# Optimization experiments

Measured on AMD Instinct MI355X. Metric: run time of the kernel, lower is better.

The kernel has to match this reference:

```python
import jax, jax.numpy as jnp
import numpy as np

B, T, C = 128, 256, 256
K1, S1, T1 = 2, 2, 128   # conv scale 1: kernel, stride, output time steps
K2, S2, T2 = 4, 4, 64    # conv scale 2
TT = T + T1 + T2         # 448, concatenated time dim fed to TriU
EPS = 1e-5


def hardswish(x):
    return x * jnp.clip(x + 3.0, 0.0, 6.0) / 6.0


def setup_inputs() -> dict:
    key = jax.random.key(0)
    ks = jax.random.split(key, 9)
    return {
        "x": jax.random.normal(ks[0], (B, T, C), jnp.float32),
        "conv_w1": jax.random.normal(ks[1], (C, C, K1), jnp.float32) * 0.05,
        "conv_b1": jax.random.normal(ks[2], (C,), jnp.float32) * 0.05,
        "conv_w2": jax.random.normal(ks[3], (C, C, K2), jnp.float32) * 0.05,
        "conv_b2": jax.random.normal(ks[4], (C,), jnp.float32) * 0.05,
        "ln1_g": jnp.ones((T1, C), jnp.float32),
        "ln1_b": jnp.zeros((T1, C), jnp.float32),
        "ln2_g": jnp.ones((T2, C), jnp.float32),
        "ln2_b": jnp.zeros((T2, C), jnp.float32),
        "triu_w1": jax.random.normal(ks[5], (TT, TT), jnp.float32) * 0.05,
        "triu_b1": jax.random.normal(ks[6], (TT,), jnp.float32) * 0.05,
        "triu_w2": jax.random.normal(ks[7], (TT, TT), jnp.float32) * 0.05,
        "triu_b2": jax.random.normal(ks[8], (TT,), jnp.float32) * 0.05,
    }


def _layernorm2(x, g, b):
    # nn.LayerNorm([ts, C]): normalize jointly over last two dims of [B, ts, C]
    mu = jnp.mean(x, axis=(-2, -1), keepdims=True)
    var = jnp.var(x, axis=(-2, -1), keepdims=True)
    return (x - mu) * jax.lax.rsqrt(var + EPS) * g + b


def _conv1d(x_bct, w, b, stride):
    # x: [B, C, T], w: [Cout, Cin, K] -> [B, Cout, T_out], VALID padding
    y = jax.lax.conv_general_dilated(
        x_bct, w, window_strides=(stride,), padding='VALID',
        dimension_numbers=('NCH', 'OIH', 'NCH'))
    return y + b[None, :, None]


def reference(x, conv_w1, conv_b1, conv_w2, conv_b2,
              ln1_g, ln1_b, ln2_g, ln2_b,
              triu_w1, triu_b1, triu_w2, triu_b2):
    xc = jnp.transpose(x, (0, 2, 1))  # [B, C, T]
    f1 = _layernorm2(jnp.transpose(_conv1d(xc, conv_w1, conv_b1, S1), (0, 2, 1)), ln1_g, ln1_b)
    f2 = _layernorm2(jnp.transpose(_conv1d(xc, conv_w2, conv_b2, S2), (0, 2, 1)), ln2_g, ln2_b)
    cat = jnp.concatenate([x, f1, f2], axis=1)  # [B, TT, C]
    # TriU network on time axis: per-step Linear(i+1,1) == upper-triangular matmul
    z = jnp.transpose(cat, (0, 2, 1))  # [B, C, TT]
    mask = jnp.triu(jnp.ones((TT, TT), z.dtype))  # M[j,i]=w_i[j] for j<=i
    z = hardswish(z @ (triu_w1 * mask) + triu_b1)
    z = z @ (triu_w2 * mask) + triu_b2
    return jnp.transpose(z, (0, 2, 1))  # [B, TT, C]
```

## Files before the change

kernel.cpp:

```cpp
#include <hip/hip_runtime.h>
#include <hip/hip_bf16.h>

#define Bn   128
#define Tn   256
#define Cn   256
#define T1n  128
#define T2n  64
#define TTn  448
#define EPSf 1e-5f

typedef __attribute__((ext_vector_type(8))) short short8;
typedef __attribute__((ext_vector_type(4))) short short4v;
typedef __attribute__((ext_vector_type(4))) float f32x4;

__device__ __forceinline__ unsigned short f2b(float f) {
    union { __hip_bfloat16 h; unsigned short u; } cv;
    cv.h = __float2bfloat16(f);
    return cv.u;
}

__device__ __forceinline__ short8 cvt8(float4 a, float4 b) {
    short8 r;
    r[0] = (short)f2b(a.x); r[1] = (short)f2b(a.y); r[2] = (short)f2b(a.z); r[3] = (short)f2b(a.w);
    r[4] = (short)f2b(b.x); r[5] = (short)f2b(b.y); r[6] = (short)f2b(b.z); r[7] = (short)f2b(b.w);
    return r;
}

__global__ __launch_bounds__(256) void prep_all(
        const float* __restrict__ cw1, const float* __restrict__ cw2,
        const float* __restrict__ tw1, const float* __restrict__ tw2,
        const float* __restrict__ ln1g, const float* __restrict__ ln1b,
        const float* __restrict__ ln2g, const float* __restrict__ ln2b,
        unsigned short* __restrict__ w1rT, unsigned short* __restrict__ w2rT,
        unsigned short* __restrict__ wm1b, unsigned short* __restrict__ wm2b,
        float* __restrict__ gt1, float* __restrict__ bt1,
        float* __restrict__ gt2, float* __restrict__ bt2) {
    int idx = blockIdx.x * 256 + threadIdx.x;
    if (idx < 131072) {
        int co = idx >> 9, r = idx & 511, k = r >> 8, ci = r & 255;
        w1rT[idx] = f2b(cw1[(size_t)co * 512 + ci * 2 + k]);
    } else if ((idx -= 131072) < 262144) {
        int co = idx >> 10, r = idx & 1023, k = r >> 8, ci = r & 255;
        w2rT[idx] = f2b(cw2[(size_t)co * 1024 + ci * 4 + k]);
    } else if ((idx -= 262144) < 200704) {
        int i = idx / TTn, j = idx % TTn;
        wm1b[idx] = (j <= i) ? f2b(tw1[(size_t)j * TTn + i]) : (unsigned short)0;
    } else if ((idx -= 200704) < 200704) {
        int i = idx / TTn, j = idx % TTn;
        wm2b[idx] = (j <= i) ? f2b(tw2[(size_t)j * TTn + i]) : (unsigned short)0;
    } else if ((idx -= 200704) < 32768) {
        int c = idx >> 7, r = idx & 127;
        gt1[idx] = ln1g[(size_t)r * Cn + c];
    } else if ((idx -= 32768) < 32768) {
        int c = idx >> 7, r = idx & 127;
        bt1[idx] = ln1b[(size_t)r * Cn + c];
    } else if ((idx -= 32768) < 16384) {
        int c = idx >> 6, r = idx & 63;
        gt2[idx] = ln2g[(size_t)r * Cn + c];
    } else if ((idx -= 16384) < 16384) {
        int c = idx >> 6, r = idx & 63;
        bt2[idx] = ln2b[(size_t)r * Cn + c];
    }
}

__global__ __launch_bounds__(256) void xpose_kernel(const float* __restrict__ x,
                                                    unsigned short* __restrict__ catb) {
    __shared__ float tl[64][65];
    int b = blockIdx.z, t0 = blockIdx.y * 64, c0 = blockIdx.x * 64;
    const float* xp = x + (size_t)b * Tn * Cn;
    int lr = threadIdx.x >> 4;
    int lc = (threadIdx.x & 15) * 4;
#pragma unroll
    for (int rr = 0; rr < 4; ++rr) {
        int row = lr + rr * 16;
        float4 v = *(const float4*)(xp + (size_t)(t0 + row) * Cn + c0 + lc);
        tl[lc + 0][row] = v.x; tl[lc + 1][row] = v.y;
        tl[lc + 2][row] = v.z; tl[lc + 3][row] = v.w;
    }
    __syncthreads();
    int cr = threadIdx.x >> 2, tq = (threadIdx.x & 3) * 16;
    unsigned short* qp = catb + (size_t)b * (TTn * Cn) + (size_t)(c0 + cr) * TTn + t0 + tq;
    short8 o0, o1;
#pragma unroll
    for (int j = 0; j < 8; ++j) {
        o0[j] = (short)f2b(tl[cr][tq + j]);
        o1[j] = (short)f2b(tl[cr][tq + 8 + j]);
    }
    *(short8*)(qp) = o0;
    *(short8*)(qp + 8) = o1;
}

__device__ __forceinline__ void conv_body(char* smem,
        const float* __restrict__ x, int lda,
        const unsigned short* __restrict__ Bw,
        const float* __restrict__ bias,
        float* __restrict__ Cout, long cstride, int ldc, int K,
        float* __restrict__ psout, int slot, int nslots,
        int m0, int n0, int bz) {
    const int tid = threadIdx.x;
    const int lane = tid & 63;
    const int wid = tid >> 6;
    const int wr = wid >> 1, wc = wid & 1;

    const int ar = tid >> 2, akq = tid & 3;
    const int bn_ = tid >> 1, bkh = (tid & 1) * 32;

    const float* Afp = x + (size_t)bz * (Tn * Cn) + (size_t)(m0 + ar) * lda + akq * 16;
    const unsigned short* Bp = Bw + (size_t)(n0 + bn_) * K + bkh;

    const int awb = ar * 128 + akq * 32;
    const int aswz = (ar & 7) << 4;
    const int bwb = bn_ * 128 + bkh * 2;
    const int bswz = (bn_ & 7) << 4;

    short8 ra0, ra1, rb0, rb1, rb2, rb3;
    auto loadA = [&](int k0) {
        const float* p = Afp + k0;
        float4 v0 = *(const float4*)(p);
        float4 v1 = *(const float4*)(p + 4);
        float4 v2 = *(const float4*)(p + 8);
        float4 v3 = *(const float4*)(p + 12);
        ra0 = cvt8(v0, v1);
        ra1 = cvt8(v2, v3);
    };
    auto loadB = [&](int k0) {
        rb0 = *(const short8*)(Bp + k0);
        rb1 = *(const short8*)(Bp + k0 + 8);
        rb2 = *(const short8*)(Bp + k0 + 16);
        rb3 = *(const short8*)(Bp + k0 + 24);
    };
    auto stage = [&](int buf) {
        char* AsB = smem + buf * 8192;
        char* BsB = smem + 16384 + buf * 16384;
        *(short8*)(AsB + ((awb) ^ aswz)) = ra0;
        *(short8*)(AsB + ((awb + 16) ^ aswz)) = ra1;
        *(short8*)(BsB + ((bwb) ^ bswz)) = rb0;
        *(short8*)(BsB + ((bwb + 16) ^ bswz)) = rb1;
        *(short8*)(BsB + ((bwb + 32) ^ bswz)) = rb2;
        *(short8*)(BsB + ((bwb + 48) ^ bswz)) = rb3;
    };

    const int fl = lane & 15;
    const int fkb = (lane >> 4) * 16;
    const int amb = (wr * 32 + fl) * 128;
    const int bnb = (wc * 64 + fl) * 128;
    const int fswz = (fl & 7) << 4;

    f32x4 acc[2][4];
#pragma unroll
    for (int i = 0; i < 2; ++i)
#pragma unroll
        for (int j = 0; j < 4; ++j) acc[i][j] = (f32x4){0.f, 0.f, 0.f, 0.f};

    const int nkt = K >> 6;
    loadA(0); loadB(0);
    stage(0);
    __syncthreads();
    for (int kt = 0; kt < nkt; ++kt) {
        const int cur = kt & 1;
        if (kt + 1 < nkt) { loadA((kt + 1) * 64); loadB((kt + 1) * 64); }
        char* AsB = smem + cur * 8192;
        char* BsB = smem + 16384 + cur * 16384;
#pragma unroll
        for (int ks = 0; ks < 2; ++ks) {
            const int kb = ks * 64 + fkb;
            short8 af0 = *(const short8*)(AsB + ((amb + kb) ^ fswz));
            short8 af1 = *(const short8*)(AsB + ((amb + 2048 + kb) ^ fswz));
            short8 bf0 = *(const short8*)(BsB + ((bnb + kb) ^ fswz));
            short8 bf1 = *(const short8*)(BsB + ((bnb + 2048 + kb) ^ fswz));
            short8 bf2 = *(const short8*)(BsB + ((bnb + 4096 + kb) ^ fswz));
            short8 bf3 = *(const short8*)(BsB + ((bnb + 6144 + kb) ^ fswz));
            acc[0][0] = __builtin_amdgcn_mfma_f32_16x16x32_bf16(af0, bf0, acc[0][0], 0, 0, 0);
            acc[0][1] = __builtin_amdgcn_mfma_f32_16x16x32_bf16(af0, bf1, acc[0][1], 0, 0, 0);
            acc[0][2] = __builtin_amdgcn_mfma_f32_16x16x32_bf16(af0, bf2, acc[0][2], 0, 0, 0);
            acc[0][3] = __builtin_amdgcn_mfma_f32_16x16x32_bf16(af0, bf3, acc[0][3], 0, 0, 0);
            acc[1][0] = __builtin_amdgcn_mfma_f32_16x16x32_bf16(af1, bf0, acc[1][0], 0, 0, 0);
            acc[1][1] = __builtin_amdgcn_mfma_f32_16x16x32_bf16(af1, bf1, acc[1][1], 0, 0, 0);
            acc[1][2] = __builtin_amdgcn_mfma_f32_16x16x32_bf16(af1, bf2, acc[1][2], 0, 0, 0);
            acc[1][3] = __builtin_amdgcn_mfma_f32_16x16x32_bf16(af1, bf3, acc[1][3], 0, 0, 0);
        }
        if (kt + 1 < nkt) stage(cur ^ 1);
        __syncthreads();
    }

    const int lrow = (lane >> 4) * 4;
    float s_ = 0.f, ss_ = 0.f;
#pragma unroll
    for (int mf = 0; mf < 2; ++mf) {
        const int trow = m0 + wr * 32 + mf * 16 + lrow;
#pragma unroll
        for (int nf = 0; nf < 4; ++nf) {
            const int col = n0 + wc * 64 + nf * 16 + fl;
            f32x4 v = acc[mf][nf];
            v += bias[col];
#pragma unroll
            for (int r = 0; r < 4; ++r) { s_ += v[r]; ss_ = fmaf(v[r], v[r], ss_); }
            float* Cb = Cout + (size_t)bz * cstride + (size_t)col * ldc + trow;
            *(f32x4*)Cb = v;
        }
    }

#pragma unroll
    for (int o = 32; o > 0; o >>= 1) { s_ += __shfl_down(s_, o); ss_ += __shfl_down(ss_, o); }
    float* rsm = (float*)smem;
    if (lane == 0) { rsm[wid] = s_; rsm[wid + 4] = ss_; }
    __syncthreads();
    if (tid == 0) {
        float S = rsm[0] + rsm[1] + rsm[2] + rsm[3];
        float SS = rsm[4] + rsm[5] + rsm[6] + rsm[7];
        psout[((size_t)bz * nslots + slot) * 2 + 0] = S;
        psout[((size_t)bz * nslots + slot) * 2 + 1] = SS;
    }
}

__global__ __launch_bounds__(256) void conv_all(
        const float* __restrict__ x,
        const unsigned short* __restrict__ w1rT, const unsigned short* __restrict__ w2rT,
        const float* __restrict__ cb1, const float* __restrict__ cb2,
        float* __restrict__ c1t, float* __restrict__ c2t,
        float* __restrict__ ps1, float* __restrict__ ps2) {
    __shared__ alignas(16) char smem[49152];
    const int y = blockIdx.y, xb = blockIdx.x, bz = blockIdx.z;
    if (y < 2) {
        conv_body(smem, x, 512, w1rT, cb1, c1t, (long)Cn * T1n, T1n, 512,
                  ps1, y * 2 + xb, 4, y * 64, xb * 128, bz);
    } else {
        conv_body(smem, x, 1024, w2rT, cb2, c2t, (long)Cn * T2n, T2n, 1024,
                  ps2, xb, 2, 0, xb * 128, bz);
    }
}

__global__ __launch_bounds__(256) void ln_apply_both(
        const float* __restrict__ c1t, const float* __restrict__ c2t,
        const float* __restrict__ gt1, const float* __restrict__ bt1,
        const float* __restrict__ gt2, const float* __restrict__ bt2,
        const float* __restrict__ ps1, const float* __restrict__ ps2,
        unsigned short* __restrict__ catb) {
    const int b = blockIdx.y, bx = blockIdx.x;
    const float *p, *g, *be;
    unsigned short* q;
    int LG, n, base;
    float S = 0.f, SS = 0.f;
    if (bx < 16) {
        n = Cn * T1n; LG = 7;
        p = c1t + (size_t)b * n; g = gt1; be = bt1;
        q = catb + (size_t)b * (TTn * Cn) + Tn;
#pragma unroll
        for (int s_ = 0; s_ < 4; ++s_) { S += ps1[b * 8 + s_ * 2]; SS += ps1[b * 8 + s_ * 2 + 1]; }
        base = bx * 2048;
    } else {
        n = Cn * T2n; LG = 6;
        p = c2t + (size_t)b * n; g = gt2; be = bt2;
        q = catb + (size_t)b * (TTn * Cn) + Tn + T1n;
#pragma unroll
        for (int s_ = 0; s_ < 2; ++s_) { S += ps2[b * 4 + s_ * 2]; SS += ps2[b * 4 + s_ * 2 + 1]; }
        base = (bx - 16) * 2048;
    }
    float mu = S / n;
    float rs = rsqrtf(SS / n - mu * mu + EPSf);

    int i = base + threadIdx.x * 8;
    int c = i >> LG, t = i & ((1 << LG) - 1);
    float4 v0 = *(const float4*)(p + i);
    float4 v1 = *(const float4*)(p + i + 4);
    float4 g0 = *(const float4*)(g + i);
    float4 g1 = *(const float4*)(g + i + 4);
    float4 b0 = *(const float4*)(be + i);
    float4 b1 = *(const float4*)(be + i + 4);
    float4 o0, o1;
    o0.x = fmaf((v0.x - mu) * rs, g0.x, b0.x);
    o0.y = fmaf((v0.y - mu) * rs, g0.y, b0.y);
    o0.z = fmaf((v0.z - mu) * rs, g0.z, b0.z);
    o0.w = fmaf((v0.w - mu) * rs, g0.w, b0.w);
    o1.x = fmaf((v1.x - mu) * rs, g1.x, b1.x);
    o1.y = fmaf((v1.y - mu) * rs, g1.y, b1.y);
    o1.z = fmaf((v1.z - mu) * rs, g1.z, b1.z);
    o1.w = fmaf((v1.w - mu) * rs, g1.w, b1.w);
    *(short8*)(q + (size_t)c * TTn + t) = cvt8(o0, o1);
}

template<int EPI>
__global__ __launch_bounds__(256)
void triu_db(const unsigned short* __restrict__ Asrc,
             const unsigned short* __restrict__ Bsrc,
             const float* __restrict__ bias,
             void* __restrict__ Cv) {
    const int tid = threadIdx.x;
    const int lane = tid & 63;
    const int wid = tid >> 6;
    const int wr = wid >> 1, wc = wid & 1;

    const int bid = blockIdx.x;
    const int xcd = bid & 7, seq = bid >> 3;
    const int m0 = (seq % 7) * 64;
    const long n0 = (long)(xcd * 32 + seq / 7) * 128;

    __shared__ unsigned short As[2][64 * 64];
    __shared__ unsigned short Bs[2][128 * 64];

    const int ar = tid >> 2, akq = tid & 3;
    const int bn_ = tid >> 1, bkh = (tid & 1) * 32;

    const unsigned short* Ap = Asrc + (size_t)(m0 + ar) * TTn + akq * 16;
    const unsigned short* Bp = Bsrc + (size_t)(n0 + bn_) * TTn + bkh;

    const int awb = ar * 128 + akq * 32;
    const int aswz = (ar & 7) << 4;
    const int bwb = bn_ * 128 + bkh * 2;
    const int bswz = (bn_ & 7) << 4;

    short8 ra0, ra1, rb[4];
    auto loadAB = [&](int k0) {
        ra0 = *(const short8*)(Ap + k0);
        ra1 = *(const short8*)(Ap + k0 + 8);
#pragma unroll
        for (int j = 0; j < 4; ++j) rb[j] = *(const short8*)(Bp + k0 + j * 8);
    };
    auto stage = [&](int buf) {
        char* AsB = (char*)As[buf];
        char* BsB = (char*)Bs[buf];
        *(short8*)(AsB + ((awb) ^ aswz)) = ra0;
        *(short8*)(AsB + ((awb + 16) ^ aswz)) = ra1;
#pragma unroll
        for (int j = 0; j < 4; ++j)
            *(short8*)(BsB + ((bwb + j * 16) ^ bswz)) = rb[j];
    };

    const int fl = lane & 15;
    const int fkb = (lane >> 4) * 16;
    const int amb = (wr * 32 + fl) * 128;
    const int bnb = (wc * 64 + fl) * 128;
    const int fswz = (fl & 7) << 4;

    f32x4 acc[2][4];
#pragma unroll
    for (int i = 0; i < 2; ++i)
#pragma unroll
        for (int j = 0; j < 4; ++j) acc[i][j] = (f32x4){0.f, 0.f, 0.f, 0.f};

    const int nkt = (m0 >> 6) + 1;

    loadAB(0);
    stage(0);
    __syncthreads();
    for (int kt = 0; kt < nkt; ++kt) {
        const int cur = kt & 1;
        if (kt + 1 < nkt) loadAB((kt + 1) * 64);
        char* AsB = (char*)As[cur];
        char* BsB = (char*)Bs[cur];
#pragma unroll
        for (int ks = 0; ks < 2; ++ks) {
            const int kb = ks * 64 + fkb;
            short8 af0 = *(const short8*)(AsB + ((amb + kb) ^ fswz));
            short8 af1 = *(const short8*)(AsB + ((amb + 2048 + kb) ^ fswz));
            short8 bf0 = *(const short8*)(BsB + ((bnb + kb) ^ fswz));
            short8 bf1 = *(const short8*)(BsB + ((bnb + 2048 + kb) ^ fswz));
            short8 bf2 = *(const short8*)(BsB + ((bnb + 4096 + kb) ^ fswz));
            short8 bf3 = *(const short8*)(BsB + ((bnb + 6144 + kb) ^ fswz));
            acc[0][0] = __builtin_amdgcn_mfma_f32_16x16x32_bf16(af0, bf0, acc[0][0], 0, 0, 0);
            acc[0][1] = __builtin_amdgcn_mfma_f32_16x16x32_bf16(af0, bf1, acc[0][1], 0, 0, 0);
            acc[0][2] = __builtin_amdgcn_mfma_f32_16x16x32_bf16(af0, bf2, acc[0][2], 0, 0, 0);
            acc[0][3] = __builtin_amdgcn_mfma_f32_16x16x32_bf16(af0, bf3, acc[0][3], 0, 0, 0);
            acc[1][0] = __builtin_amdgcn_mfma_f32_16x16x32_bf16(af1, bf0, acc[1][0], 0, 0, 0);
            acc[1][1] = __builtin_amdgcn_mfma_f32_16x16x32_bf16(af1, bf1, acc[1][1], 0, 0, 0);
            acc[1][2] = __builtin_amdgcn_mfma_f32_16x16x32_bf16(af1, bf2, acc[1][2], 0, 0, 0);
            acc[1][3] = __builtin_amdgcn_mfma_f32_16x16x32_bf16(af1, bf3, acc[1][3], 0, 0, 0);
        }
        if (kt + 1 < nkt) stage(cur ^ 1);
        __syncthreads();
    }

    const int lrow = (lane >> 4) * 4;
#pragma unroll
    for (int mf = 0; mf < 2; ++mf) {
        const int trow = m0 + wr * 32 + mf * 16 + lrow;
        f32x4 bv = *(const f32x4*)(bias + trow);
#pragma unroll
        for (int nf = 0; nf < 4; ++nf) {
            const long coln = n0 + wc * 64 + nf * 16 + fl;
            f32x4 v = acc[mf][nf] + bv;
            if (EPI == 1) {
                unsigned short* Cb = (unsigned short*)Cv + (size_t)coln * TTn + trow;
                short4v pk;
#pragma unroll
                for (int r = 0; r < 4; ++r) {
                    float t = v[r];
                    float u = fminf(fmaxf(t + 3.f, 0.f), 6.f);
                    t = t * u * (1.f / 6.f);
                    pk[r] = (short)f2b(t);
                }
                *(short4v*)Cb = pk;
            } else {
                const int b = (int)(coln >> 8), c = (int)(coln & 255);
                float* Cb = (float*)Cv + ((size_t)b * TTn + trow) * Cn + c;
#pragma unroll
                for (int r = 0; r < 4; ++r) Cb[(size_t)r * Cn] = v[r];
            }
        }
    }
}

extern "C" void kernel_launch(void* const* d_in, const int* in_sizes, int n_in,
                              void* d_out, int out_size, void* d_ws, size_t ws_size,
                              hipStream_t stream) {
    const float* x    = (const float*)d_in[0];
    const float* cw1  = (const float*)d_in[1];
    const float* cb1  = (const float*)d_in[2];
    const float* cw2  = (const float*)d_in[3];
    const float* cb2  = (const float*)d_in[4];
    const float* ln1g = (const float*)d_in[5];
    const float* ln1b = (const float*)d_in[6];
    const float* ln2g = (const float*)d_in[7];
    const float* ln2b = (const float*)d_in[8];
    const float* tw1  = (const float*)d_in[9];
    const float* tb1  = (const float*)d_in[10];
    const float* tw2  = (const float*)d_in[11];
    const float* tb2  = (const float*)d_in[12];
    float* out = (float*)d_out;

    char* w = (char*)d_ws;
    unsigned short* catb = (unsigned short*)w;
    unsigned short* z1b  = (unsigned short*)(w + 29360128);
    float*          c1t  = (float*)(w + 58720256);
    float*          c2t  = (float*)(w + 75497472);
    unsigned short* w1rT = (unsigned short*)(w + 83886080);
    unsigned short* w2rT = (unsigned short*)(w + 84148224);
    unsigned short* wm1b = (unsigned short*)(w + 84672512);
    unsigned short* wm2b = (unsigned short*)(w + 85073920);
    float*          gt1  = (float*)(w + 85475328);
    float*          bt1  = (float*)(w + 85606400);
    float*          gt2  = (float*)(w + 85737472);
    float*          bt2  = (float*)(w + 85803008);
    float*          ps1  = (float*)(w + 85868544);
    float*          ps2  = (float*)(w + 85872640);

    prep_all<<<3488, 256, 0, stream>>>(cw1, cw2, tw1, tw2, ln1g, ln1b, ln2g, ln2b,
                                       w1rT, w2rT, wm1b, wm2b, gt1, bt1, gt2, bt2);

    xpose_kernel<<<dim3(4, 4, Bn), 256, 0, stream>>>(x, catb);

    conv_all<<<dim3(2, 3, Bn), 256, 0, stream>>>(x, w1rT, w2rT, cb1, cb2, c1t, c2t, ps1, ps2);

    ln_apply_both<<<dim3(24, Bn), 256, 0, stream>>>(c1t, c2t, gt1, bt1, gt2, bt2, ps1, ps2, catb);

    triu_db<1><<<1792, 256, 0, stream>>>(wm1b, catb, tb1, z1b);

    triu_db<2><<<1792, 256, 0, stream>>>(wm2b, z1b, tb2, out);
}
```

Before: 99.11 us.

## Fuse all stages into one persistent cooperative kernel with grid syncs

Replaces six separate kernel launches with one cooperative persistent kernel that loops over virtual block indices for each stage and separates the stages with grid-wide barriers. The goal is to remove per-launch overhead and inter-kernel gaps. In exchange, occupancy is capped by the shared 48KB smem and the launch-bounds hint, the triu GEMM and conv units now run with a limited resident grid and lose the XCD mapping implied by hardware block order, and device property queries are added on the host side of every launch.

Result: slower. 266.6 us (+169.0%).

```diff
diff --git a/kernel.cpp b/kernel.cpp
--- a/kernel.cpp
+++ b/kernel.cpp
@@ -1,5 +1,8 @@
 #include <hip/hip_runtime.h>
 #include <hip/hip_bf16.h>
+#include <hip/hip_cooperative_groups.h>
+
+namespace cg = cooperative_groups;
 
 #define Bn   128
 #define Tn   256
@@ -13,6 +16,13 @@
 typedef __attribute__((ext_vector_type(4))) short short4v;
 typedef __attribute__((ext_vector_type(4))) float f32x4;
 
+struct Params {
+    const float *x, *cw1, *cb1, *cw2, *cb2, *ln1g, *ln1b, *ln2g, *ln2b, *tw1, *tb1, *tw2, *tb2;
+    float* out;
+    unsigned short *catb, *z1b, *w1rT, *w2rT, *wm1b, *wm2b;
+    float *c1t, *c2t, *gt1, *bt1, *gt2, *bt2, *ps1, *ps2;
+};
+
 __device__ __forceinline__ unsigned short f2b(float f) {
     union { __hip_bfloat16 h; unsigned short u; } cv;
     cv.h = __float2bfloat16(f);
@@ -26,48 +36,40 @@
     return r;
 }
 
-__global__ __launch_bounds__(256) void prep_all(
-        const float* __restrict__ cw1, const float* __restrict__ cw2,
-        const float* __restrict__ tw1, const float* __restrict__ tw2,
-        const float* __restrict__ ln1g, const float* __restrict__ ln1b,
-        const float* __restrict__ ln2g, const float* __restrict__ ln2b,
-        unsigned short* __restrict__ w1rT, unsigned short* __restrict__ w2rT,
-        unsigned short* __restrict__ wm1b, unsigned short* __restrict__ wm2b,
-        float* __restrict__ gt1, float* __restrict__ bt1,
-        float* __restrict__ gt2, float* __restrict__ bt2) {
-    int idx = blockIdx.x * 256 + threadIdx.x;
+__device__ void prep_step(const Params& P, int vb) {
+    int idx = vb * 256 + threadIdx.x;
     if (idx < 131072) {
         int co = idx >> 9, r = idx & 511, k = r >> 8, ci = r & 255;
-        w1rT[idx] = f2b(cw1[(size_t)co * 512 + ci * 2 + k]);
+        P.w1rT[idx] = f2b(P.cw1[(size_t)co * 512 + ci * 2 + k]);
     } else if ((idx -= 131072) < 262144) {
         int co = idx >> 10, r = idx & 1023, k = r >> 8, ci = r & 255;
-        w2rT[idx] = f2b(cw2[(size_t)co * 1024 + ci * 4 + k]);
+        P.w2rT[idx] = f2b(P.cw2[(size_t)co * 1024 + ci * 4 + k]);
     } else if ((idx -= 262144) < 200704) {
         int i = idx / TTn, j = idx % TTn;
-        wm1b[idx] = (j <= i) ? f2b(tw1[(size_t)j * TTn + i]) : (unsigned short)0;
+        P.wm1b[idx] = (j <= i) ? f2b(P.tw1[(size_t)j * TTn + i]) : (unsigned short)0;
     } else if ((idx -= 200704) < 200704) {
         int i = idx / TTn, j = idx % TTn;
-        wm2b[idx] = (j <= i) ? f2b(tw2[(size_t)j * TTn + i]) : (unsigned short)0;
+        P.wm2b[idx] = (j <= i) ? f2b(P.tw2[(size_t)j * TTn + i]) : (unsigned short)0;
     } else if ((idx -= 200704) < 32768) {
         int c = idx >> 7, r = idx & 127;
-        gt1[idx] = ln1g[(size_t)r * Cn + c];
+        P.gt1[idx] = P.ln1g[(size_t)r * Cn + c];
     } else if ((idx -= 32768) < 32768) {
         int c = idx >> 7, r = idx & 127;
-        bt1[idx] = ln1b[(size_t)r * Cn + c];
+        P.bt1[idx] = P.ln1b[(size_t)r * Cn + c];
     } else if ((idx -= 32768) < 16384) {
         int c = idx >> 6, r = idx & 63;
-        gt2[idx] = ln2g[(size_t)r * Cn + c];
+        P.gt2[idx] = P.ln2g[(size_t)r * Cn + c];
     } else if ((idx -= 16384) < 16384) {
         int c = idx >> 6, r = idx & 63;
-        bt2[idx] = ln2b[(size_t)r * Cn + c];
-    }
-}
-
-__global__ __launch_bounds__(256) void xpose_kernel(const float* __restrict__ x,
-                                                    unsigned short* __restrict__ catb) {
-    __shared__ float tl[64][65];
-    int b = blockIdx.z, t0 = blockIdx.y * 64, c0 = blockIdx.x * 64;
-    const float* xp = x + (size_t)b * Tn * Cn;
+        P.bt2[idx] = P.ln2b[(size_t)r * Cn + c];
+    }
+}
+
+__device__ void xpose_tile(char* smem, const Params& P, int vb) {
+    float (*tl)[65] = (float(*)[65])smem;
+    int b = vb >> 4, r = vb & 15;
+    int t0 = (r >> 2) * 64, c0 = (r & 3) * 64;
+    const float* xp = P.x + (size_t)b * Tn * Cn;
     int lr = threadIdx.x >> 4;
     int lc = (threadIdx.x & 15) * 4;
 #pragma unroll
@@ -79,7 +81,7 @@
     }
     __syncthreads();
     int cr = threadIdx.x >> 2, tq = (threadIdx.x & 3) * 16;
-    unsigned short* qp = catb + (size_t)b * (TTn * Cn) + (size_t)(c0 + cr) * TTn + t0 + tq;
+    unsigned short* qp = P.catb + (size_t)b * (TTn * Cn) + (size_t)(c0 + cr) * TTn + t0 + tq;
     short8 o0, o1;
 #pragma unroll
     for (int j = 0; j < 8; ++j) {
@@ -90,7 +92,7 @@
     *(short8*)(qp + 8) = o1;
 }
 
-__device__ __forceinline__ void conv_body(char* smem,
+__device__ void conv_body(char* smem,
         const float* __restrict__ x, int lda,
         const unsigned short* __restrict__ Bw,
         const float* __restrict__ bias,
@@ -211,49 +213,40 @@
         psout[((size_t)bz * nslots + slot) * 2 + 0] = S;
         psout[((size_t)bz * nslots + slot) * 2 + 1] = SS;
     }
-}
-
-__global__ __launch_bounds__(256) void conv_all(
-        const float* __restrict__ x,
-        const unsigned short* __restrict__ w1rT, const unsigned short* __restrict__ w2rT,
-        const float* __restrict__ cb1, const float* __restrict__ cb2,
-        float* __restrict__ c1t, float* __restrict__ c2t,
-        float* __restrict__ ps1, float* __restrict__ ps2) {
-    __shared__ alignas(16) char smem[49152];
-    const int y = blockIdx.y, xb = blockIdx.x, bz = blockIdx.z;
-    if (y < 2) {
-        conv_body(smem, x, 512, w1rT, cb1, c1t, (long)Cn * T1n, T1n, 512,
-                  ps1, y * 2 + xb, 4, y * 64, xb * 128, bz);
+    __syncthreads();
+}
+
+__device__ void conv_unit(char* smem, const Params& P, int vb) {
+    const int bz = vb & 127;
+    const int u = vb >> 7;
+    if (u < 4) {
+        conv_body(smem, P.x, 512, P.w1rT, P.cb1, P.c1t, (long)Cn * T1n, T1n, 512,
+                  P.ps1, u, 4, (u >> 1) * 64, (u & 1) * 128, bz);
     } else {
-        conv_body(smem, x, 1024, w2rT, cb2, c2t, (long)Cn * T2n, T2n, 1024,
-                  ps2, xb, 2, 0, xb * 128, bz);
-    }
-}
-
-__global__ __launch_bounds__(256) void ln_apply_both(
-        const float* __restrict__ c1t, const float* __restrict__ c2t,
-        const float* __restrict__ gt1, const float* __restrict__ bt1,
-        const float* __restrict__ gt2, const float* __restrict__ bt2,
-        const float* __restrict__ ps1, const float* __restrict__ ps2,
-        unsigned short* __restrict__ catb) {
-    const int b = blockIdx.y, bx = blockIdx.x;
+        conv_body(smem, P.x, 1024, P.w2rT, P.cb2, P.c2t, (long)Cn * T2n, T2n, 1024,
+                  P.ps2, u - 4, 2, 0, (u - 4) * 128, bz);
+    }
+}
+
+__device__ void ln_unit(const Params& P, int vb) {
+    const int bx = vb % 24, b = vb / 24;
     const float *p, *g, *be;
     unsigned short* q;
     int LG, n, base;
     float S = 0.f, SS = 0.f;
     if (bx < 16) {
         n = Cn * T1n; LG = 7;
-        p = c1t + (size_t)b * n; g = gt1; be = bt1;
-        q = catb + (size_t)b * (TTn * Cn) + Tn;
-#pragma unroll
-        for (int s_ = 0; s_ < 4; ++s_) { S += ps1[b * 8 + s_ * 2]; SS += ps1[b * 8 + s_ * 2 + 1]; }
+        p = P.c1t + (size_t)b * n; g = P.gt1; be = P.bt1;
+        q = P.catb + (size_t)b * (TTn * Cn) + Tn;
+#pragma unroll
+        for (int s_ = 0; s_ < 4; ++s_) { S += P.ps1[b * 8 + s_ * 2]; SS += P.ps1[b * 8 + s_ * 2 + 1]; }
         base = bx * 2048;
     } else {
         n = Cn * T2n; LG = 6;
-        p = c2t + (size_t)b * n; g = gt2; be = bt2;
-        q = catb + (size_t)b * (TTn * Cn) + Tn + T1n;
-#pragma unroll
-        for (int s_ = 0; s_ < 2; ++s_) { S += ps2[b * 4 + s_ * 2]; SS += ps2[b * 4 + s_ * 2 + 1]; }
+        p = P.c2t + (size_t)b * n; g = P.gt2; be = P.bt2;
+        q = P.catb + (size_t)b * (TTn * Cn) + Tn + T1n;
+#pragma unroll
+        for (int s_ = 0; s_ < 2; ++s_) { S += P.ps2[b * 4 + s_ * 2]; SS += P.ps2[b * 4 + s_ * 2 + 1]; }
         base = (bx - 16) * 2048;
     }
     float mu = S / n;
@@ -280,23 +273,19 @@
 }
 
 template<int EPI>
-__global__ __launch_bounds__(256)
-void triu_db(const unsigned short* __restrict__ Asrc,
-             const unsigned short* __restrict__ Bsrc,
-             const float* __restrict__ bias,
-             void* __restrict__ Cv) {
+__device__ void triu_unit(char* smem,
+                          const unsigned short* __restrict__ Asrc,
+                          const unsigned short* __restrict__ Bsrc,
+                          const float* __restrict__ bias,
+                          void* __restrict__ Cv, int vb) {
     const int tid = threadIdx.x;
     const int lane = tid & 63;
     const int wid = tid >> 6;
     const int wr = wid >> 1, wc = wid & 1;
 
-    const int bid = blockIdx.x;
-    const int xcd = bid & 7, seq = bid >> 3;
+    const int xcd = vb & 7, seq = vb >> 3;
     const int m0 = (seq % 7) * 64;
     const long n0 = (long)(xcd * 32 + seq / 7) * 128;
-
-    __shared__ unsigned short As[2][64 * 64];
-    __shared__ unsigned short Bs[2][128 * 64];
 
     const int ar = tid >> 2, akq = tid & 3;
     const int bn_ = tid >> 1, bkh = (tid & 1) * 32;
@@ -317,8 +306,8 @@
         for (int j = 0; j < 4; ++j) rb[j] = *(const short8*)(Bp + k0 + j * 8);
     };
     auto stage = [&](int buf) {
-        char* AsB = (char*)As[buf];
-        char* BsB = (char*)Bs[buf];
+        char* AsB = smem + buf * 8192;
+        char* BsB = smem + 16384 + buf * 16384;
         *(short8*)(AsB + ((awb) ^ aswz)) = ra0;
         *(short8*)(AsB + ((awb + 16) ^ aswz)) = ra1;
 #pragma unroll
@@ -346,8 +335,8 @@
     for (int kt = 0; kt < nkt; ++kt) {
         const int cur = kt & 1;
         if (kt + 1 < nkt) loadAB((kt + 1) * 64);
-        char* AsB = (char*)As[cur];
-        char* BsB = (char*)Bs[cur];
+        char* AsB = smem + cur * 8192;
+        char* BsB = smem + 16384 + cur * 16384;
 #pragma unroll
         for (int ks = 0; ks < 2; ++ks) {
             const int kb = ks * 64 + fkb;
@@ -400,50 +389,74 @@
     }
 }
 
+__global__ __launch_bounds__(256, 3) void fused_all(Params P) {
+    __shared__ alignas(16) char smem[49152];
+    cg::grid_group grid = cg::this_grid();
+    const int G = gridDim.x, bid = blockIdx.x;
+
+    for (int vb = bid; vb < 3488; vb += G) prep_step(P, vb);
+    for (int vb = bid; vb < 2048; vb += G) { xpose_tile(smem, P, vb); __syncthreads(); }
+    grid.sync();
+
+    for (int vb = bid; vb < 768; vb += G) conv_unit(smem, P, vb);
+    grid.sync();
+
+    for (int vb = bid; vb < 3072; vb += G) ln_unit(P, vb);
+    grid.sync();
+
+    for (int vb = bid; vb < 1792; vb += G) triu_unit<1>(smem, P.wm1b, P.catb, P.tb1, P.z1b, vb);
+    grid.sync();
+
+    for (int vb = bid; vb < 1792; vb += G) triu_unit<2>(smem, P.wm2b, P.z1b, P.tb2, P.out, vb);
+}
+
 extern "C" void kernel_launch(void* const* d_in, const int* in_sizes, int n_in,
                               void* d_out, int out_size, void* d_ws, size_t ws_size,
                               hipStream_t stream) {
-    const float* x    = (const float*)d_in[0];
-    const float* cw1  = (const float*)d_in[1];
-    const float* cb1  = (const float*)d_in[2];
-    const float* cw2  = (const float*)d_in[3];
-    const float* cb2  = (const float*)d_in[4];
-    const float* ln1g = (const float*)d_in[5];
-    const float* ln1b = (const float*)d_in[6];
-    const float* ln2g = (const float*)d_in[7];
-    const float* ln2b = (const float*)d_in[8];
-    const float* tw1  = (const float*)d_in[9];
-    const float* tb1  = (const float*)d_in[10];
-    const float* tw2  = (const float*)d_in[11];
-    const float* tb2  = (const float*)d_in[12];
-    float* out = (float*)d_out;
-
     char* w = (char*)d_ws;
-    unsigned short* catb = (unsigned short*)w;
-    unsigned short* z1b  = (unsigned short*)(w + 29360128);
-    float*          c1t  = (float*)(w + 58720256);
-    float*          c2t  = (float*)(w + 75497472);
-    unsigned short* w1rT = (unsigned short*)(w + 83886080);
-    unsigned short* w2rT = (unsigned short*)(w + 84148224);
-    unsigned short* wm1b = (unsigned short*)(w + 84672512);
-    unsigned short* wm2b = (unsigned short*)(w + 85073920);
-    float*          gt1  = (float*)(w + 85475328);
-    float*          bt1  = (float*)(w + 85606400);
-    float*          gt2  = (float*)(w + 85737472);
-    float*          bt2  = (float*)(w + 85803008);
-    float*          ps1  = (float*)(w + 85868544);
-    float*          ps2  = (float*)(w + 85872640);
-
-    prep_all<<<3488, 256, 0, stream>>>(cw1, cw2, tw1, tw2, ln1g, ln1b, ln2g, ln2b,
-                                       w1rT, w2rT, wm1b, wm2b, gt1, bt1, gt2, bt2);
-
-    xpose_kernel<<<dim3(4, 4, Bn), 256, 0, stream>>>(x, catb);
-
-    conv_all<<<dim3(2, 3, Bn), 256, 0, stream>>>(x, w1rT, w2rT, cb1, cb2, c1t, c2t, ps1, ps2);
-
-    ln_apply_both<<<dim3(24, Bn), 256, 0, stream>>>(c1t, c2t, gt1, bt1, gt2, bt2, ps1, ps2, catb);
-
-    triu_db<1><<<1792, 256, 0, stream>>>(wm1b, catb, tb1, z1b);
-
-    triu_db<2><<<1792, 256, 0, stream>>>(wm2b, z1b, tb2, out);
-}
+    Params P;
+    P.x    = (const float*)d_in[0];
+    P.cw1  = (const float*)d_in[1];
+    P.cb1  = (const float*)d_in[2];
+    P.cw2  = (const float*)d_in[3];
+    P.cb2  = (const float*)d_in[4];
+    P.ln1g = (const float*)d_in[5];
+    P.ln1b = (const float*)d_in[6];
+    P.ln2g = (const float*)d_in[7];
+    P.ln2b = (const float*)d_in[8];
+    P.tw1  = (const float*)d_in[9];
+    P.tb1  = (const float*)d_in[10];
+    P.tw2  = (const float*)d_in[11];
+    P.tb2  = (const float*)d_in[12];
+    P.out  = (float*)d_out;
+    P.catb = (unsigned short*)w;
+    P.z1b  = (unsigned short*)(w + 29360128);
+    P.c1t  = (float*)(w + 58720256);
+    P.c2t  = (float*)(w + 75497472);
+    P.w1rT = (unsigned short*)(w + 83886080);
+    P.w2rT = (unsigned short*)(w + 84148224);
+    P.wm1b = (unsigned short*)(w + 84672512);
+    P.wm2b = (unsigned short*)(w + 85073920);
+    P.gt1  = (float*)(w + 85475328);
+    P.bt1  = (float*)(w + 85606400);
+    P.gt2  = (float*)(w + 85737472);
+    P.bt2  = (float*)(w + 85803008);
+    P.ps1  = (float*)(w + 85868544);
+    P.ps2  = (float*)(w + 85872640);
+
+    int perCU = 0;
+    hipOccupancyMaxActiveBlocksPerMultiprocessor(&perCU, fused_all, 256, 0);
+    if (perCU < 1) perCU = 1;
+    int nCU = 256;
+    hipDeviceProp_t prop;
+    int dev = 0;
+    if (hipGetDevice(&dev) == hipSuccess && hipGetDeviceProperties(&prop, dev) == hipSuccess)
+        nCU = prop.multiProcessorCount;
+    long grid = (long)perCU * nCU;
+    if (grid > 768) grid = 768;
+    grid &= ~7L;
+    if (grid < 8) grid = 8;
+
+    void* kargs[] = { (void*)&P };
+    hipLaunchCooperativeKernel((const void*)fused_all, dim3((unsigned)grid), dim3(256), kargs, 0, stream);
+}
```
